# Optimization experiments

Measured on AMD Instinct MI355X. Metric: run time of the kernel, lower is better.

## Reference

```python
import jax, jax.numpy as jnp
import numpy as np

EPS = 1e-7
N_NODES = 100000

# --- Lorentz model (c = 1), working at the origin o = (1, 0, ..., 0) ---

def expmap0(v_spatial):
    """Exp map at origin: tangent spatial part [N, d] -> hyperboloid point [N, d+1]."""
    nrm = jnp.sqrt(jnp.maximum(jnp.sum(v_spatial * v_spatial, axis=-1, keepdims=True), EPS))
    x0 = jnp.cosh(nrm)
    xs = jnp.sinh(nrm) / nrm * v_spatial
    return jnp.concatenate([x0, xs], axis=-1)


def logmap0(x):
    """Log map at origin: point [N, d+1] -> tangent spatial part [N, d]."""
    x0 = jnp.maximum(x[..., :1], 1.0 + EPS)
    xs = x[..., 1:]
    nrm = jnp.sqrt(jnp.maximum(jnp.sum(xs * xs, axis=-1, keepdims=True), EPS))
    return jnp.arccosh(x0) / nrm * xs


def sigmoid_nonlin(x):
    # log map -> sigmoid in tangent space -> exp map (c_in = c_out = 1)
    return expmap0(jax.nn.sigmoid(logmap0(x)))


def hgcn_layer(x, edge_index, W, b):
    """HGCN conv: tangent-space linear + mean aggregation over edges + exp map."""
    t = logmap0(x)                      # [N, d_in]
    h = t @ W + b                       # [N, d_out]
    src, dst = edge_index[0], edge_index[1]
    msg = h[src]                        # [E, d_out] gather
    agg = jax.ops.segment_sum(msg, dst, num_segments=N_NODES)
    deg = jax.ops.segment_sum(jnp.ones((edge_index.shape[1],), h.dtype), dst,
                              num_segments=N_NODES)
    agg = agg / jnp.maximum(deg, 1.0)[:, None]
    return expmap0(agg)


def setup_inputs() -> dict:
    key = jax.random.key(0)
    ks = jax.random.split(key, 10)
    d_in, h1, h2, h_mlp, d_out = 64, 64, 64, 128, 40
    return {
        "features": jax.random.normal(ks[0], (N_NODES, d_in), jnp.float32),
        "edge_index": jax.random.randint(ks[1], (2, 1600000), 0, N_NODES, jnp.int64),
        "W1": jax.random.normal(ks[2], (d_in, h1), jnp.float32) * 0.05,
        "b1": jnp.zeros((h1,), jnp.float32),
        "W2": jax.random.normal(ks[3], (h1, h2), jnp.float32) * 0.05,
        "b2": jnp.zeros((h2,), jnp.float32),
        "W3": jax.random.normal(ks[4], (h2, h_mlp), jnp.float32) * 0.05,
        "b3": jnp.zeros((h_mlp,), jnp.float32),
        "W4": jax.random.normal(ks[5], (h_mlp, d_out), jnp.float32) * 0.05,
        "b4": jnp.zeros((d_out,), jnp.float32),
    }


def reference(features, edge_index, W1, b1, W2, b2, W3, b3, W4, b4):
    # lift Euclidean features to the hyperboloid (pad time coord, exp map)
    x = expmap0(features)                       # [N, d_in+1]
    x = hgcn_layer(x, edge_index, W1, b1)
    x = sigmoid_nonlin(x)
    x = hgcn_layer(x, edge_index, W2, b2)
    x = sigmoid_nonlin(x)
    t = logmap0(x)                              # [N, h2] (spatial part, drops time coord)
    # MLP head (dropout inactive at eval)
    h = jax.nn.relu(t @ W3 + b3)
    return h @ W4 + b4
```

## Files before the change

kernel.cpp:

```cpp
#include <hip/hip_runtime.h>


constexpr int CSHIFT = 9;
constexpr int CNODES = 1 << CSHIFT;
constexpr int EPB    = 4096;
constexpr int EPT    = EPB / 256;
constexpr int CAP    = 16384;

constexpr int W1F_OFF = 0;
constexpr int W2F_OFF = 4096;
constexpr int W3F_OFF = 8192;
constexpr int W4F_OFF = 16384;
constexpr int WIMG_TOT = 22528;

typedef __attribute__((ext_vector_type(8))) short short8;
typedef __attribute__((ext_vector_type(4))) float floatx4;

__device__ __forceinline__ float sigmoidf(float x) {
    return 1.0f / (1.0f + __expf(-x));
}
__device__ __forceinline__ unsigned short f2bf(float f) {
    unsigned int u = __float_as_uint(f);
    u = (u + 0x7FFFu + ((u >> 16) & 1u)) >> 16;
    return (unsigned short)u;
}

__global__ __launch_bounds__(256) void part_prep_k(
    const int* __restrict__ src, const int* __restrict__ dst,
    int* __restrict__ ccur, int* __restrict__ arena, int E, int NBUCK, int gP,
    const float* __restrict__ feat, unsigned short* __restrict__ featbf,
    const float* __restrict__ W1, const float* __restrict__ W2,
    const float* __restrict__ W3, const float* __restrict__ W4,
    unsigned short* __restrict__ img, int n8)
{
    __shared__ int  hist[256];
    __shared__ int  exoff[256];
    __shared__ int  lcur[256];
    __shared__ int  gbase[256];
    __shared__ int  stage[EPB];
    __shared__ unsigned char stageB[EPB];

    const int tid = threadIdx.x;

    if ((int)blockIdx.x >= gP) {
        int i = ((int)blockIdx.x - gP) * 256 + tid;
        if (i < n8) {
            const float4* p = (const float4*)feat + (size_t)i * 2;
            float4 a = p[0], b = p[1];
            uint4 o;
            o.x = (unsigned)f2bf(a.x) | ((unsigned)f2bf(a.y) << 16);
            o.y = (unsigned)f2bf(a.z) | ((unsigned)f2bf(a.w) << 16);
            o.z = (unsigned)f2bf(b.x) | ((unsigned)f2bf(b.y) << 16);
            o.w = (unsigned)f2bf(b.z) | ((unsigned)f2bf(b.w) << 16);
            ((uint4*)featbf)[i] = o;
            return;
        }
        int t = i - n8;
        if (t >= WIMG_TOT) return;
        float v = 0.f;
        int s = t;
        if (s < W2F_OFF) {
            int j = s & 7, m = (s >> 3) & 15, q = (s >> 7) & 3, kk = (s >> 9) & 1, c = s >> 10;
            v = W1[(kk * 32 + q * 8 + j) * 64 + c * 16 + m];
        } else if (s < W3F_OFF) {
            s -= W2F_OFF;
            int j = s & 7, m = (s >> 3) & 15, q = (s >> 7) & 3, kk = (s >> 9) & 1, c = s >> 10;
            v = W2[(kk * 32 + q * 8 + j) * 64 + c * 16 + m];
        } else if (s < W4F_OFF) {
            s -= W3F_OFF;
            int j = s & 7, m = (s >> 3) & 15, q = (s >> 7) & 3, kk = (s >> 9) & 1, c = s >> 10;
            v = W3[(kk * 32 + q * 8 + j) * 128 + c * 16 + m];
        } else {
            s -= W4F_OFF;
            int j = s & 7, m = (s >> 3) & 15, q = (s >> 7) & 3, kk = (s >> 9) & 3, c = s >> 11;
            int n = c * 16 + m;
            if (n < 40) v = W4[(kk * 32 + q * 8 + j) * 40 + n];
        }
        img[t] = f2bf(v);
        return;
    }

    const int e0  = blockIdx.x * EPB;
    const int ec  = min(EPB, E - e0);

    int pk[EPT], bk[EPT];
    hist[tid] = 0;
    __syncthreads();
    #pragma unroll
    for (int j = 0; j < EPT; j++) {
        int idx = tid + j * 256;
        if (idx < ec) {
            int s = src[e0 + idx];
            int d = dst[e0 + idx];
            bk[j] = d >> CSHIFT;
            pk[j] = s | ((d & (CNODES - 1)) << 17);
            atomicAdd(&hist[bk[j]], 1);
        } else bk[j] = -1;
    }
    __syncthreads();
    const int h = hist[tid];
    exoff[tid] = h;
    __syncthreads();
    for (int dd = 1; dd < 256; dd <<= 1) {
        int v = 0;
        if (tid >= dd) v = exoff[tid - dd];
        __syncthreads();
        if (tid >= dd) exoff[tid] += v;
        __syncthreads();
    }
    const int ex = exoff[tid] - h;
    int gb = 0;
    if (tid < NBUCK && h > 0) gb = atomicAdd(ccur + tid, h);
    __syncthreads();
    exoff[tid] = ex;
    lcur[tid]  = ex;
    gbase[tid] = gb;
    __syncthreads();
    #pragma unroll
    for (int j = 0; j < EPT; j++) {
        if (bk[j] >= 0) {
            int l = atomicAdd(&lcur[bk[j]], 1);
            stage[l]  = pk[j];
            stageB[l] = (unsigned char)bk[j];
        }
    }
    __syncthreads();
    for (int i = tid; i < ec; i += 256) {
        int b = stageB[i];
        arena[(size_t)b * CAP + gbase[b] + (i - exoff[b])] = stage[i];
    }
}

__global__ __launch_bounds__(1024) void csr_fine(const int* __restrict__ arena,
                                                 const int* __restrict__ ccur,
                                                 int* __restrict__ off,
                                                 int* __restrict__ ssrc,
                                                 int N, int E, int NBUCK) {
    __shared__ int part[256];
    __shared__ int cnt[CNODES];
    __shared__ int cur[CNODES];
    __shared__ int wpre[8];
    const int b = blockIdx.x;
    const int node0 = b << CSHIFT;
    const int tid = threadIdx.x;
    const int lane = tid & 63, wid = tid >> 6;

    if (tid < 256) part[tid] = (tid < NBUCK) ? ccur[tid] : 0;
    __syncthreads();
    for (int d = 1; d < 256; d <<= 1) {
        int v = 0;
        if (tid < 256 && tid >= d) v = part[tid - d];
        __syncthreads();
        if (tid < 256 && tid >= d) part[tid] += v;
        __syncthreads();
    }
    const int cbeg = (b > 0) ? part[b - 1] : 0;
    const int ec   = min(ccur[b], CAP);
    if (b == 0 && tid == 0) off[N] = E;

    if (tid < CNODES) cnt[tid] = 0;
    __syncthreads();
    const int* pe = arena + (size_t)b * CAP;
    for (int i = tid; i < ec; i += 1024)
        atomicAdd(&cnt[(pe[i] >> 17) & (CNODES - 1)], 1);
    __syncthreads();

    int c = (tid < CNODES) ? cnt[tid] : 0;
    int v = c;
    #pragma unroll
    for (int d = 1; d < 64; d <<= 1) {
        int t = __shfl_up(v, d);
        if (lane >= d) v += t;
    }
    if (tid < CNODES && lane == 63) wpre[wid] = v;
    __syncthreads();
    if (tid == 0) {
        int s = 0;
        #pragma unroll
        for (int k = 0; k < CNODES / 64; k++) { int t = wpre[k]; wpre[k] = s; s += t; }
    }
    __syncthreads();
    if (tid < CNODES) {
        int ex = wpre[wid] + v - c;
        cur[tid] = ex;
        int node = node0 + tid;
        if (node < N) off[node] = cbeg + ex;
    }
    __syncthreads();
    for (int i = tid; i < ec; i += 1024) {
        int p = pe[i];
        int pos = cbeg + atomicAdd(&cur[(p >> 17) & (CNODES - 1)], 1);
        ssrc[pos] = p & 0x1FFFF;
    }
}

#define ACC8(v)                                    \
    acc[0] += __uint_as_float((v).x << 16);        \
    acc[1] += __uint_as_float((v).x & 0xFFFF0000u);\
    acc[2] += __uint_as_float((v).y << 16);        \
    acc[3] += __uint_as_float((v).y & 0xFFFF0000u);\
    acc[4] += __uint_as_float((v).z << 16);        \
    acc[5] += __uint_as_float((v).z & 0xFFFF0000u);\
    acc[6] += __uint_as_float((v).w << 16);        \
    acc[7] += __uint_as_float((v).w & 0xFFFF0000u);

__device__ __forceinline__ void gather_tile_wave(
    const unsigned short* __restrict__ h, const int* __restrict__ off,
    const int* __restrict__ ssrc, unsigned short* Agg, int rowB, int N,
    int w, int lane)
{
    #pragma unroll
    for (int pass = 0; pass < 2; pass++) {
        int rl = w * 16 + pass * 8 + (lane >> 3);
        int g  = rowB + rl;
        int q  = (lane & 7) * 8;
        uint4 p = make_uint4(0u, 0u, 0u, 0u);
        if (g < N) {
            int beg = off[g], end = off[g + 1];
            float acc[8] = {0.f, 0.f, 0.f, 0.f, 0.f, 0.f, 0.f, 0.f};
            int i = beg;
            for (; i + 8 <= end; i += 8) {
                uint4 v0 = *(const uint4*)(h + (size_t)ssrc[i]     * 64 + q);
                uint4 v1 = *(const uint4*)(h + (size_t)ssrc[i + 1] * 64 + q);
                uint4 v2 = *(const uint4*)(h + (size_t)ssrc[i + 2] * 64 + q);
                uint4 v3 = *(const uint4*)(h + (size_t)ssrc[i + 3] * 64 + q);
                uint4 v4 = *(const uint4*)(h + (size_t)ssrc[i + 4] * 64 + q);
                uint4 v5 = *(const uint4*)(h + (size_t)ssrc[i + 5] * 64 + q);
                uint4 v6 = *(const uint4*)(h + (size_t)ssrc[i + 6] * 64 + q);
                uint4 v7 = *(const uint4*)(h + (size_t)ssrc[i + 7] * 64 + q);
                ACC8(v0); ACC8(v1); ACC8(v2); ACC8(v3);
                ACC8(v4); ACC8(v5); ACC8(v6); ACC8(v7);
            }
            for (; i + 2 <= end; i += 2) {
                uint4 v0 = *(const uint4*)(h + (size_t)ssrc[i]     * 64 + q);
                uint4 v1 = *(const uint4*)(h + (size_t)ssrc[i + 1] * 64 + q);
                ACC8(v0); ACC8(v1);
            }
            for (; i < end; i++) {
                uint4 v = *(const uint4*)(h + (size_t)ssrc[i] * 64 + q);
                ACC8(v);
            }
            float inv = __builtin_amdgcn_rcpf((float)max(end - beg, 1));
            p.x = (unsigned)f2bf(acc[0]*inv) | ((unsigned)f2bf(acc[1]*inv) << 16);
            p.y = (unsigned)f2bf(acc[2]*inv) | ((unsigned)f2bf(acc[3]*inv) << 16);
            p.z = (unsigned)f2bf(acc[4]*inv) | ((unsigned)f2bf(acc[5]*inv) << 16);
            p.w = (unsigned)f2bf(acc[6]*inv) | ((unsigned)f2bf(acc[7]*inv) << 16);
        }
        *(uint4*)(Agg + rl * 72 + q) = p;
    }
}

__global__ __launch_bounds__(128) void aggemm1_k(
    const unsigned short* __restrict__ featbf, const int* __restrict__ off,
    const int* __restrict__ ssrc, const unsigned short* __restrict__ img,
    const float* __restrict__ bias, unsigned short* __restrict__ t1, int N)
{
    __shared__ alignas(16) unsigned short Agg[32 * 72];

    const int tid = threadIdx.x;
    const int rowB = blockIdx.x * 32;
    const int w = tid >> 6, lane = tid & 63;
    const int m = lane & 15, quad = lane >> 4;
    const int row0 = rowB + w * 16;

    gather_tile_wave(featbf, off, ssrc, Agg, rowB, N, w, lane);

    const short8* Wf = (const short8*)(img + W1F_OFF);
    floatx4 acc[4];
    #pragma unroll
    for (int c = 0; c < 4; c++) acc[c] = (floatx4){0.f, 0.f, 0.f, 0.f};
    #pragma unroll
    for (int kk = 0; kk < 2; kk++) {
        short8 a = *(const short8*)(Agg + (w * 16 + m) * 72 + kk * 32 + quad * 8);
        #pragma unroll
        for (int c = 0; c < 4; c++) {
            short8 b = Wf[((c * 2 + kk) * 4 + quad) * 16 + m];
            acc[c] = __builtin_amdgcn_mfma_f32_16x16x32_bf16(a, b, acc[c], 0, 0, 0);
        }
    }
    bool dzr[4];
    int rows[4];
    #pragma unroll
    for (int r = 0; r < 4; r++) {
        rows[r] = row0 + quad * 4 + r;
        dzr[r] = (rows[r] < N) ? (off[rows[r] + 1] == off[rows[r]]) : false;
    }
    #pragma unroll
    for (int c = 0; c < 4; c++) {
        int col = c * 16 + m;
        float bv = bias[col];
        #pragma unroll
        for (int r = 0; r < 4; r++) {
            if (rows[r] < N) {
                float v = dzr[r] ? 0.5f : sigmoidf(acc[c][r] + bv);
                t1[(size_t)rows[r] * 64 + col] = f2bf(v);
            }
        }
    }
}

__global__ __launch_bounds__(128) void aggep3_k(
    const unsigned short* __restrict__ t1, const int* __restrict__ off,
    const int* __restrict__ ssrc, const unsigned short* __restrict__ img,
    const float* __restrict__ b2, const float* __restrict__ b3,
    const float* __restrict__ b4, float* __restrict__ out, int N)
{
    __shared__ alignas(16) unsigned short SM[4608];
    unsigned short* T2  = SM;
    unsigned short* Agg = SM + 2304;
    unsigned short* H3h = SM + 2304;

    const int tid = threadIdx.x;
    const int rowB = blockIdx.x * 32;
    const int w = tid >> 6, lane = tid & 63;
    const int m = lane & 15, quad = lane >> 4;
    const int row0 = rowB + w * 16;

    gather_tile_wave(t1, off, ssrc, Agg, rowB, N, w, lane);

    {
        const short8* Wf = (const short8*)(img + W2F_OFF);
        floatx4 acc[4];
        #pragma unroll
        for (int c = 0; c < 4; c++) acc[c] = (floatx4){0.f, 0.f, 0.f, 0.f};
        #pragma unroll
        for (int kk = 0; kk < 2; kk++) {
            short8 a = *(const short8*)(Agg + (w * 16 + m) * 72 + kk * 32 + quad * 8);
            #pragma unroll
            for (int c = 0; c < 4; c++) {
                short8 b = Wf[((c * 2 + kk) * 4 + quad) * 16 + m];
                acc[c] = __builtin_amdgcn_mfma_f32_16x16x32_bf16(a, b, acc[c], 0, 0, 0);
            }
        }
        bool dzr[4];
        #pragma unroll
        for (int r = 0; r < 4; r++) {
            int row = row0 + quad * 4 + r;
            dzr[r] = (row < N) ? (off[row + 1] == off[row]) : false;
        }
        #pragma unroll
        for (int c = 0; c < 4; c++) {
            int col = c * 16 + m;
            float bv = b2[col];
            #pragma unroll
            for (int r = 0; r < 4; r++) {
                int rl = w * 16 + quad * 4 + r;
                float v = dzr[r] ? 0.5f : sigmoidf(acc[c][r] + bv);
                T2[rl * 72 + col] = f2bf(v);
            }
        }
    }

    floatx4 acc2[3];
    #pragma unroll
    for (int c = 0; c < 3; c++) acc2[c] = (floatx4){0.f, 0.f, 0.f, 0.f};
    const short8* Wf3 = (const short8*)(img + W3F_OFF);
    const short8* Wf4 = (const short8*)(img + W4F_OFF);

    #pragma unroll
    for (int half = 0; half < 2; half++) {
        floatx4 acc[4];
        #pragma unroll
        for (int c = 0; c < 4; c++) acc[c] = (floatx4){0.f, 0.f, 0.f, 0.f};
        #pragma unroll
        for (int kk = 0; kk < 2; kk++) {
            short8 a = *(const short8*)(T2 + (w * 16 + m) * 72 + kk * 32 + quad * 8);
            #pragma unroll
            for (int c = 0; c < 4; c++) {
                short8 b = Wf3[(((half * 4 + c) * 2 + kk) * 4 + quad) * 16 + m];
                acc[c] = __builtin_amdgcn_mfma_f32_16x16x32_bf16(a, b, acc[c], 0, 0, 0);
            }
        }
        #pragma unroll
        for (int c = 0; c < 4; c++) {
            int col = c * 16 + m;
            float bv = b3[half * 64 + col];
            #pragma unroll
            for (int r = 0; r < 4; r++) {
                int rl = w * 16 + quad * 4 + r;
                H3h[rl * 72 + col] = f2bf(fmaxf(acc[c][r] + bv, 0.f));
            }
        }
        #pragma unroll
        for (int kk2 = 0; kk2 < 2; kk2++) {
            short8 a = *(const short8*)(H3h + (w * 16 + m) * 72 + kk2 * 32 + quad * 8);
            #pragma unroll
            for (int c = 0; c < 3; c++) {
                short8 b = Wf4[((c * 4 + half * 2 + kk2) * 4 + quad) * 16 + m];
                acc2[c] = __builtin_amdgcn_mfma_f32_16x16x32_bf16(a, b, acc2[c], 0, 0, 0);
            }
        }
    }

    #pragma unroll
    for (int c = 0; c < 3; c++) {
        int col = c * 16 + m;
        if (col < 40) {
            float bv = b4[col];
            #pragma unroll
            for (int r = 0; r < 4; r++) {
                int row = row0 + quad * 4 + r;
                if (row < N) out[(size_t)row * 40 + col] = acc2[c][r] + bv;
            }
        }
    }
}

extern "C" void kernel_launch(void* const* d_in, const int* in_sizes, int n_in,
                              void* d_out, int out_size, void* d_ws, size_t ws_size,
                              hipStream_t stream)
{
    const float* feat = (const float*)d_in[0];
    const int*   eidx = (const int*)d_in[1];
    const float* W1 = (const float*)d_in[2];
    const float* b1 = (const float*)d_in[3];
    const float* W2 = (const float*)d_in[4];
    const float* b2 = (const float*)d_in[5];
    const float* W3 = (const float*)d_in[6];
    const float* b3 = (const float*)d_in[7];
    const float* W4 = (const float*)d_in[8];
    const float* b4 = (const float*)d_in[9];

    const int N = in_sizes[0] / 64;
    const int E = in_sizes[1] / 2;
    const int* src = eidx;
    const int* dst = eidx + E;

    const int NBUCK = (N + CNODES - 1) / CNODES;

    unsigned short* featbf = (unsigned short*)d_ws;
    unsigned short* t1     = featbf + (size_t)N * 64;
    unsigned short* img    = t1     + (size_t)N * 64;
    int*   off   = (int*)(img + WIMG_TOT);
    int*   ccur  = off + (N + 1);
    int*   ssrc  = ccur + NBUCK;
    int*   arena = ssrc + E;
    float* out   = (float*)d_out;

    hipMemsetAsync(ccur, 0, (size_t)NBUCK * sizeof(int), stream);

    const dim3 blk(256);
    const int gP  = (E + EPB - 1) / EPB;
    const int g32 = (N + 31) / 32;
    const int n8  = N * 64 / 8;
    const int gPC = (n8 + WIMG_TOT + 255) / 256;

    part_prep_k<<<gP + gPC, blk, 0, stream>>>(src, dst, ccur, arena, E, NBUCK,
                                              gP, feat, featbf, W1, W2, W3, W4,
                                              img, n8);
    csr_fine<<<NBUCK, dim3(1024), 0, stream>>>(arena, ccur, off, ssrc, N, E, NBUCK);

    aggemm1_k<<<g32, dim3(128), 0, stream>>>(featbf, off, ssrc, img, b1, t1, N);
    aggep3_k<<<g32, dim3(128), 0, stream>>>(t1, off, ssrc, img, b2, b3, b4, out, N);
}
```

Before: 219.1 us.

## Replace bucketed two-pass CSR build with degree-count, scan, atomic scatter

New measurement: 367.3 us. +67.6%, slower.

```diff
diff --git a/kernel.cpp b/kernel.cpp
--- a/kernel.cpp
+++ b/kernel.cpp
@@ -1,11 +1,7 @@
 #include <hip/hip_runtime.h>
 
 
-constexpr int CSHIFT = 9;
-constexpr int CNODES = 1 << CSHIFT;
-constexpr int EPB    = 4096;
-constexpr int EPT    = EPB / 256;
-constexpr int CAP    = 16384;
+constexpr int SCAN_B = 1024;
 
 constexpr int W1F_OFF = 0;
 constexpr int W2F_OFF = 4096;
@@ -25,173 +21,135 @@
     return (unsigned short)u;
 }
 
-__global__ __launch_bounds__(256) void part_prep_k(
-    const int* __restrict__ src, const int* __restrict__ dst,
-    int* __restrict__ ccur, int* __restrict__ arena, int E, int NBUCK, int gP,
+__global__ __launch_bounds__(256) void prep_deg_k(
+    const int* __restrict__ dst, int* __restrict__ deg, int E, int gA,
     const float* __restrict__ feat, unsigned short* __restrict__ featbf,
     const float* __restrict__ W1, const float* __restrict__ W2,
     const float* __restrict__ W3, const float* __restrict__ W4,
     unsigned short* __restrict__ img, int n8)
 {
-    __shared__ int  hist[256];
-    __shared__ int  exoff[256];
-    __shared__ int  lcur[256];
-    __shared__ int  gbase[256];
-    __shared__ int  stage[EPB];
-    __shared__ unsigned char stageB[EPB];
-
-    const int tid = threadIdx.x;
-
-    if ((int)blockIdx.x >= gP) {
-        int i = ((int)blockIdx.x - gP) * 256 + tid;
-        if (i < n8) {
-            const float4* p = (const float4*)feat + (size_t)i * 2;
-            float4 a = p[0], b = p[1];
-            uint4 o;
-            o.x = (unsigned)f2bf(a.x) | ((unsigned)f2bf(a.y) << 16);
-            o.y = (unsigned)f2bf(a.z) | ((unsigned)f2bf(a.w) << 16);
-            o.z = (unsigned)f2bf(b.x) | ((unsigned)f2bf(b.y) << 16);
-            o.w = (unsigned)f2bf(b.z) | ((unsigned)f2bf(b.w) << 16);
-            ((uint4*)featbf)[i] = o;
-            return;
-        }
-        int t = i - n8;
-        if (t >= WIMG_TOT) return;
-        float v = 0.f;
-        int s = t;
-        if (s < W2F_OFF) {
-            int j = s & 7, m = (s >> 3) & 15, q = (s >> 7) & 3, kk = (s >> 9) & 1, c = s >> 10;
-            v = W1[(kk * 32 + q * 8 + j) * 64 + c * 16 + m];
-        } else if (s < W3F_OFF) {
-            s -= W2F_OFF;
-            int j = s & 7, m = (s >> 3) & 15, q = (s >> 7) & 3, kk = (s >> 9) & 1, c = s >> 10;
-            v = W2[(kk * 32 + q * 8 + j) * 64 + c * 16 + m];
-        } else if (s < W4F_OFF) {
-            s -= W3F_OFF;
-            int j = s & 7, m = (s >> 3) & 15, q = (s >> 7) & 3, kk = (s >> 9) & 1, c = s >> 10;
-            v = W3[(kk * 32 + q * 8 + j) * 128 + c * 16 + m];
-        } else {
-            s -= W4F_OFF;
-            int j = s & 7, m = (s >> 3) & 15, q = (s >> 7) & 3, kk = (s >> 9) & 3, c = s >> 11;
-            int n = c * 16 + m;
-            if (n < 40) v = W4[(kk * 32 + q * 8 + j) * 40 + n];
-        }
-        img[t] = f2bf(v);
+    const int tid = threadIdx.x;
+
+    if ((int)blockIdx.x < gA) {
+        const int base = blockIdx.x * 2048;
+        int dv[8];
+        #pragma unroll
+        for (int k = 0; k < 8; k++) {
+            int id = base + tid + k * 256;
+            dv[k] = (id < E) ? dst[id] : -1;
+        }
+        #pragma unroll
+        for (int k = 0; k < 8; k++)
+            if (dv[k] >= 0) atomicAdd(&deg[dv[k]], 1);
         return;
     }
 
-    const int e0  = blockIdx.x * EPB;
-    const int ec  = min(EPB, E - e0);
-
-    int pk[EPT], bk[EPT];
-    hist[tid] = 0;
-    __syncthreads();
-    #pragma unroll
-    for (int j = 0; j < EPT; j++) {
-        int idx = tid + j * 256;
-        if (idx < ec) {
-            int s = src[e0 + idx];
-            int d = dst[e0 + idx];
-            bk[j] = d >> CSHIFT;
-            pk[j] = s | ((d & (CNODES - 1)) << 17);
-            atomicAdd(&hist[bk[j]], 1);
-        } else bk[j] = -1;
-    }
-    __syncthreads();
-    const int h = hist[tid];
-    exoff[tid] = h;
-    __syncthreads();
-    for (int dd = 1; dd < 256; dd <<= 1) {
-        int v = 0;
-        if (tid >= dd) v = exoff[tid - dd];
-        __syncthreads();
-        if (tid >= dd) exoff[tid] += v;
-        __syncthreads();
-    }
-    const int ex = exoff[tid] - h;
-    int gb = 0;
-    if (tid < NBUCK && h > 0) gb = atomicAdd(ccur + tid, h);
-    __syncthreads();
-    exoff[tid] = ex;
-    lcur[tid]  = ex;
-    gbase[tid] = gb;
-    __syncthreads();
-    #pragma unroll
-    for (int j = 0; j < EPT; j++) {
-        if (bk[j] >= 0) {
-            int l = atomicAdd(&lcur[bk[j]], 1);
-            stage[l]  = pk[j];
-            stageB[l] = (unsigned char)bk[j];
-        }
-    }
-    __syncthreads();
-    for (int i = tid; i < ec; i += 256) {
-        int b = stageB[i];
-        arena[(size_t)b * CAP + gbase[b] + (i - exoff[b])] = stage[i];
-    }
-}
-
-__global__ __launch_bounds__(1024) void csr_fine(const int* __restrict__ arena,
-                                                 const int* __restrict__ ccur,
-                                                 int* __restrict__ off,
-                                                 int* __restrict__ ssrc,
-                                                 int N, int E, int NBUCK) {
-    __shared__ int part[256];
-    __shared__ int cnt[CNODES];
-    __shared__ int cur[CNODES];
-    __shared__ int wpre[8];
-    const int b = blockIdx.x;
-    const int node0 = b << CSHIFT;
+    int i = ((int)blockIdx.x - gA) * 256 + tid;
+    if (i < n8) {
+        const float4* p = (const float4*)feat + (size_t)i * 2;
+        float4 a = p[0], b = p[1];
+        uint4 o;
+        o.x = (unsigned)f2bf(a.x) | ((unsigned)f2bf(a.y) << 16);
+        o.y = (unsigned)f2bf(a.z) | ((unsigned)f2bf(a.w) << 16);
+        o.z = (unsigned)f2bf(b.x) | ((unsigned)f2bf(b.y) << 16);
+        o.w = (unsigned)f2bf(b.z) | ((unsigned)f2bf(b.w) << 16);
+        ((uint4*)featbf)[i] = o;
+        return;
+    }
+    int t = i - n8;
+    if (t >= WIMG_TOT) return;
+    float v = 0.f;
+    int s = t;
+    if (s < W2F_OFF) {
+        int j = s & 7, m = (s >> 3) & 15, q = (s >> 7) & 3, kk = (s >> 9) & 1, c = s >> 10;
+        v = W1[(kk * 32 + q * 8 + j) * 64 + c * 16 + m];
+    } else if (s < W3F_OFF) {
+        s -= W2F_OFF;
+        int j = s & 7, m = (s >> 3) & 15, q = (s >> 7) & 3, kk = (s >> 9) & 1, c = s >> 10;
+        v = W2[(kk * 32 + q * 8 + j) * 64 + c * 16 + m];
+    } else if (s < W4F_OFF) {
+        s -= W3F_OFF;
+        int j = s & 7, m = (s >> 3) & 15, q = (s >> 7) & 3, kk = (s >> 9) & 1, c = s >> 10;
+        v = W3[(kk * 32 + q * 8 + j) * 128 + c * 16 + m];
+    } else {
+        s -= W4F_OFF;
+        int j = s & 7, m = (s >> 3) & 15, q = (s >> 7) & 3, kk = (s >> 9) & 3, c = s >> 11;
+        int n = c * 16 + m;
+        if (n < 40) v = W4[(kk * 32 + q * 8 + j) * 40 + n];
+    }
+    img[t] = f2bf(v);
+}
+
+__global__ __launch_bounds__(SCAN_B) void scan1_k(
+    const int* __restrict__ deg, int* __restrict__ off,
+    int* __restrict__ bsum, int N)
+{
+    __shared__ int wsum[16];
+    __shared__ int wpre[16];
     const int tid = threadIdx.x;
     const int lane = tid & 63, wid = tid >> 6;
-
-    if (tid < 256) part[tid] = (tid < NBUCK) ? ccur[tid] : 0;
-    __syncthreads();
-    for (int d = 1; d < 256; d <<= 1) {
-        int v = 0;
-        if (tid < 256 && tid >= d) v = part[tid - d];
-        __syncthreads();
-        if (tid < 256 && tid >= d) part[tid] += v;
-        __syncthreads();
-    }
-    const int cbeg = (b > 0) ? part[b - 1] : 0;
-    const int ec   = min(ccur[b], CAP);
-    if (b == 0 && tid == 0) off[N] = E;
-
-    if (tid < CNODES) cnt[tid] = 0;
-    __syncthreads();
-    const int* pe = arena + (size_t)b * CAP;
-    for (int i = tid; i < ec; i += 1024)
-        atomicAdd(&cnt[(pe[i] >> 17) & (CNODES - 1)], 1);
-    __syncthreads();
-
-    int c = (tid < CNODES) ? cnt[tid] : 0;
-    int v = c;
-    #pragma unroll
-    for (int d = 1; d < 64; d <<= 1) {
-        int t = __shfl_up(v, d);
-        if (lane >= d) v += t;
-    }
-    if (tid < CNODES && lane == 63) wpre[wid] = v;
+    const int i = blockIdx.x * SCAN_B + tid;
+
+    int d = (i < N) ? deg[i] : 0;
+    int v = d;
+    #pragma unroll
+    for (int k = 1; k < 64; k <<= 1) {
+        int t = __shfl_up(v, k);
+        if (lane >= k) v += t;
+    }
+    if (lane == 63) wsum[wid] = v;
     __syncthreads();
     if (tid == 0) {
         int s = 0;
         #pragma unroll
-        for (int k = 0; k < CNODES / 64; k++) { int t = wpre[k]; wpre[k] = s; s += t; }
+        for (int k = 0; k < 16; k++) { int t = wsum[k]; wpre[k] = s; s += t; }
+        bsum[blockIdx.x] = s;
     }
     __syncthreads();
-    if (tid < CNODES) {
-        int ex = wpre[wid] + v - c;
-        cur[tid] = ex;
-        int node = node0 + tid;
-        if (node < N) off[node] = cbeg + ex;
+    if (i < N) off[i] = wpre[wid] + v - d;
+}
+
+__global__ __launch_bounds__(SCAN_B) void scan2_k(
+    const int* __restrict__ bsum, int* __restrict__ off,
+    int* __restrict__ cur, int N, int E)
+{
+    __shared__ int bpre_s;
+    const int tid = threadIdx.x;
+    if (tid == 0) {
+        int s = 0;
+        for (int k = 0; k < (int)blockIdx.x; k++) s += bsum[k];
+        bpre_s = s;
     }
     __syncthreads();
-    for (int i = tid; i < ec; i += 1024) {
-        int p = pe[i];
-        int pos = cbeg + atomicAdd(&cur[(p >> 17) & (CNODES - 1)], 1);
-        ssrc[pos] = p & 0x1FFFF;
-    }
+    const int i = blockIdx.x * SCAN_B + tid;
+    if (i < N) {
+        int o = off[i] + bpre_s;
+        off[i] = o;
+        cur[i] = o;
+    }
+    if (blockIdx.x == 0 && tid == 0) off[N] = E;
+}
+
+__global__ __launch_bounds__(256) void scatter_k(
+    const int* __restrict__ src, const int* __restrict__ dst,
+    int* __restrict__ cur, int* __restrict__ ssrc, int E)
+{
+    const int tid = threadIdx.x;
+    const int base = blockIdx.x * 2048;
+    int sv[8], dv[8];
+    #pragma unroll
+    for (int k = 0; k < 8; k++) {
+        int id = base + tid + k * 256;
+        if (id < E) { sv[k] = src[id]; dv[k] = dst[id]; }
+        else dv[k] = -1;
+    }
+    int pos[8];
+    #pragma unroll
+    for (int k = 0; k < 8; k++)
+        if (dv[k] >= 0) pos[k] = atomicAdd(&cur[dv[k]], 1);
+    #pragma unroll
+    for (int k = 0; k < 8; k++)
+        if (dv[k] >= 0) ssrc[pos[k]] = sv[k];
 }
 
 #define ACC8(v)                                    \
@@ -426,29 +384,28 @@
     const int* src = eidx;
     const int* dst = eidx + E;
 
-    const int NBUCK = (N + CNODES - 1) / CNODES;
-
     unsigned short* featbf = (unsigned short*)d_ws;
     unsigned short* t1     = featbf + (size_t)N * 64;
     unsigned short* img    = t1     + (size_t)N * 64;
     int*   off   = (int*)(img + WIMG_TOT);
-    int*   ccur  = off + (N + 1);
-    int*   ssrc  = ccur + NBUCK;
-    int*   arena = ssrc + E;
+    int*   cur   = off + (N + 1);
+    int*   bsum  = cur + N;
+    int*   ssrc  = bsum + 128;
     float* out   = (float*)d_out;
 
-    hipMemsetAsync(ccur, 0, (size_t)NBUCK * sizeof(int), stream);
-
-    const dim3 blk(256);
-    const int gP  = (E + EPB - 1) / EPB;
-    const int g32 = (N + 31) / 32;
+    const int gA  = (E + 2047) / 2048;
     const int n8  = N * 64 / 8;
     const int gPC = (n8 + WIMG_TOT + 255) / 256;
-
-    part_prep_k<<<gP + gPC, blk, 0, stream>>>(src, dst, ccur, arena, E, NBUCK,
-                                              gP, feat, featbf, W1, W2, W3, W4,
-                                              img, n8);
-    csr_fine<<<NBUCK, dim3(1024), 0, stream>>>(arena, ccur, off, ssrc, N, E, NBUCK);
+    const int gS  = (N + SCAN_B - 1) / SCAN_B;
+    const int g32 = (N + 31) / 32;
+
+    hipMemsetAsync(cur, 0, (size_t)N * sizeof(int), stream);
+    prep_deg_k<<<gA + gPC, dim3(256), 0, stream>>>(dst, cur, E, gA, feat,
+                                                   featbf, W1, W2, W3, W4,
+                                                   img, n8);
+    scan1_k<<<gS, dim3(SCAN_B), 0, stream>>>(cur, off, bsum, N);
+    scan2_k<<<gS, dim3(SCAN_B), 0, stream>>>(bsum, off, cur, N, E);
+    scatter_k<<<gA, dim3(256), 0, stream>>>(src, dst, cur, ssrc, E);
 
     aggemm1_k<<<g32, dim3(128), 0, stream>>>(featbf, off, ssrc, img, b1, t1, N);
     aggep3_k<<<g32, dim3(128), 0, stream>>>(t1, off, ssrc, img, b2, b3, b4, out, N);
```
